# Optimization experiments

Hardware: AMD Instinct MI355X
Metric: run time of the kernel (lower is better)

The kernel has to match this reference:

```python
import jax, jax.numpy as jnp
import numpy as np

HEADS = 20  # head_dim = 1280 // 20 = 64
LORA_SCALE = 1.0


def setup_inputs() -> dict:
    key = jax.random.key(0)
    ks = jax.random.split(key, 16)
    B, S, C, R = 2, 2048, 1280, 4
    w = 0.02  # keep activations numerically tame
    inp = {
        "x": jax.random.normal(ks[0], (B, S, C), jnp.float32),
        "Wq": jax.random.normal(ks[1], (C, C), jnp.float32) * w,
        "Wk": jax.random.normal(ks[2], (C, C), jnp.float32) * w,
        "Wv": jax.random.normal(ks[3], (C, C), jnp.float32) * w,
        "Wo": jax.random.normal(ks[4], (C, C), jnp.float32) * w,
        "bo": jnp.zeros((C,), jnp.float32),
        "Aq": jax.random.normal(ks[5], (R, C), jnp.float32) * w,
        "Bq": jax.random.normal(ks[6], (C, R), jnp.float32) * w,
        "Ak": jax.random.normal(ks[7], (R, C), jnp.float32) * w,
        "Bk": jax.random.normal(ks[8], (C, R), jnp.float32) * w,
        "Av": jax.random.normal(ks[9], (R, C), jnp.float32) * w,
        "Bv": jax.random.normal(ks[10], (C, R), jnp.float32) * w,
        "Ao": jax.random.normal(ks[11], (R, C), jnp.float32) * w,
        "Bo": jax.random.normal(ks[12], (C, R), jnp.float32) * w,
    }
    return inp


def _lora(x, A, B):
    # LoRALinearLayer: up(down(x)); network_alpha=None -> no extra scaling
    return (x @ A.T) @ B.T


def reference(x, Wq, Wk, Wv, Wo, bo, Aq, Bq, Ak, Bk, Av, Bv, Ao, Bo):
    B, S, C = x.shape
    H = HEADS
    D = C // H
    # base projections + LoRA updates (self-attention: encoder_hidden_states = x)
    q = x @ Wq.T + LORA_SCALE * _lora(x, Aq, Bq)
    k = x @ Wk.T + LORA_SCALE * _lora(x, Ak, Bk)
    v = x @ Wv.T + LORA_SCALE * _lora(x, Av, Bv)
    # head split: [B, S, H, D]
    q = q.reshape(B, S, H, D)
    k = k.reshape(B, S, H, D)
    v = v.reshape(B, S, H, D)
    # explicit scores + softmax (attn.get_attention_scores), scale = 1/sqrt(D)
    scale = 1.0 / jnp.sqrt(jnp.asarray(D, x.dtype))
    scores = jnp.einsum("bshd,bthd->bhst", q, k) * scale  # [B, H, S, S]
    probs = jax.nn.softmax(scores, axis=-1)
    ctx = jnp.einsum("bhst,bthd->bshd", probs, v).reshape(B, S, C)
    # output projection (+bias) + LoRA; dropout is identity at eval
    out = ctx @ Wo.T + bo + LORA_SCALE * _lora(ctx, Ao, Bo)
    return out
```

## Files before the change

kernel.cpp:

```cpp
#include <hip/hip_runtime.h>

#define BATCH 2
#define SEQ   2048
#define CH    1280
#define NH    20
#define HD    64
#define BS    (BATCH*SEQ)
#define RK    4

typedef __attribute__((ext_vector_type(2)))  float floatx2;
typedef __attribute__((ext_vector_type(4)))  short bf16x4;
typedef __attribute__((ext_vector_type(8)))  short bf16x8;
typedef __attribute__((ext_vector_type(16))) float floatx16;

__device__ __forceinline__ floatx16 mfma32(bf16x8 a, bf16x8 b, floatx16 c) {
    return __builtin_amdgcn_mfma_f32_32x32x16_bf16(a, b, c, 0, 0, 0);
}
__device__ __forceinline__ floatx16 mfma32k8(bf16x4 a, bf16x4 b, floatx16 c) {
    return __builtin_amdgcn_mfma_f32_32x32x8bf16_1k(a, b, c, 0, 0, 0);
}

__device__ __forceinline__ unsigned short f2bf(float f) {
    unsigned int u = __float_as_uint(f);
    u += 0x7fffu + ((u >> 16) & 1u);
    return (unsigned short)(u >> 16);
}
__device__ __forceinline__ unsigned int packbf(float hi, float lo) {
    unsigned int a = __float_as_uint(hi) + 0x8000u;
    unsigned int b = __float_as_uint(lo) + 0x8000u;
    return __builtin_amdgcn_perm(a, b, 0x07060302u);
}
__device__ __forceinline__ float fexp2(float x) {
#if __has_builtin(__builtin_amdgcn_exp2f)
    return __builtin_amdgcn_exp2f(x);
#else
    return exp2f(x);
#endif
}

__device__ __forceinline__ void cp16(const unsigned short* g, unsigned short* l) {
    __builtin_amdgcn_global_load_lds(
        (const __attribute__((address_space(1))) unsigned int*)g,
        (__attribute__((address_space(3))) unsigned int*)l, 16, 0, 0);
}

#define FOLD_BLOCKS (CH * CH / 256)
#define CAST_BLOCKS (BS * CH / 1024)

__global__ __launch_bounds__(256) void prep(
    const float* __restrict__ x,
    const float* __restrict__ Wq, const float* __restrict__ Wk,
    const float* __restrict__ Wv, const float* __restrict__ Wo,
    const float* __restrict__ Aq, const float* __restrict__ Bq,
    const float* __restrict__ Ak, const float* __restrict__ Bk,
    const float* __restrict__ Av, const float* __restrict__ Bv,
    const float* __restrict__ Ao, const float* __restrict__ Bo,
    unsigned short* __restrict__ wq_bf, unsigned short* __restrict__ wk_bf,
    unsigned short* __restrict__ wv_bf, unsigned short* __restrict__ wo_bf,
    unsigned short* __restrict__ xb)
{
    const int bx = blockIdx.x;
    if (bx < 4 * FOLD_BLOCKS) {
        int which = bx / FOLD_BLOCKS;
        int e = (bx % FOLD_BLOCKS) * 256 + threadIdx.x;
        int i = e / CH, j = e % CH;
        const float *W, *A, *Bm;
        unsigned short* o;
        if (which == 0)      { W = Wq; A = Aq; Bm = Bq; o = wq_bf; }
        else if (which == 1) { W = Wk; A = Ak; Bm = Bk; o = wk_bf; }
        else if (which == 2) { W = Wv; A = Av; Bm = Bv; o = wv_bf; }
        else                 { W = Wo; A = Ao; Bm = Bo; o = wo_bf; }
        float acc = W[e];
#pragma unroll
        for (int r = 0; r < RK; r++) acc += Bm[i * RK + r] * A[r * CH + j];
        o[e] = f2bf(acc);
    } else {
        int idx = ((bx - 4 * FOLD_BLOCKS) * 256 + threadIdx.x) * 4;
        float4 v = *(const float4*)(x + idx);
        ushort4 o;
        o.x = f2bf(v.x); o.y = f2bf(v.y); o.z = f2bf(v.z); o.w = f2bf(v.w);
        *(ushort4*)(xb + idx) = o;
    }
}

template<bool OUTF>
__device__ __forceinline__ void gemm128(
    const unsigned short* __restrict__ A, const unsigned short* __restrict__ B,
    unsigned short* __restrict__ obf, float* __restrict__ of,
    const float* __restrict__ bias, float oscale)
{
    __shared__ __align__(16) unsigned short sa[128 * 64];
    __shared__ __align__(16) unsigned short sb[128 * 64];
    const int tid = threadIdx.x;
    const int wav = tid >> 6, lane = tid & 63;
    const int n32 = lane & 31, half = lane >> 5;
    const int wr = wav >> 1, wc = wav & 1;
    const int M0 = blockIdx.y * 128, N0 = blockIdx.x * 128;

    const unsigned short* ga[4]; const unsigned short* gb[4];
    unsigned short* la[4]; unsigned short* lb[4];
#pragma unroll
    for (int g = 0; g < 4; g++) {
        int s = g * 256 + tid;
        int row = s >> 3, cc = (s & 7) ^ (row & 7);
        ga[g] = A + (size_t)(M0 + row) * CH + cc * 8;
        gb[g] = B + (size_t)(N0 + row) * CH + cc * 8;
        la[g] = sa + (size_t)(g * 256 + wav * 64) * 8;
        lb[g] = sb + (size_t)(g * 256 + wav * 64) * 8;
    }

    const int arow0 = wr * 64 + n32, brow0 = wc * 64 + n32;

    floatx16 acc[2][2];
#pragma unroll
    for (int mt = 0; mt < 2; mt++)
#pragma unroll
        for (int nt = 0; nt < 2; nt++)
#pragma unroll
            for (int r = 0; r < 16; r++) acc[mt][nt][r] = 0.f;

    for (int k0 = 0; k0 < CH; k0 += 64) {
#pragma unroll
        for (int g = 0; g < 4; g++) { cp16(ga[g], la[g]); cp16(gb[g], lb[g]); }
#pragma unroll
        for (int g = 0; g < 4; g++) { ga[g] += 64; gb[g] += 64; }
        __syncthreads();

        bf16x8 av[2][4], bv[2][4];
#pragma unroll
        for (int mt = 0; mt < 2; mt++) {
            const int ar = arow0 + mt * 32, br = brow0 + mt * 32;
#pragma unroll
            for (int ks = 0; ks < 4; ks++) {
                const int cc = ks * 2 + half;
                av[mt][ks] = *(const bf16x8*)(sa + ar * 64 + ((cc ^ (ar & 7)) << 3));
                bv[mt][ks] = *(const bf16x8*)(sb + br * 64 + ((cc ^ (br & 7)) << 3));
            }
        }
#pragma unroll
        for (int ks = 0; ks < 4; ks++)
#pragma unroll
            for (int mt = 0; mt < 2; mt++)
#pragma unroll
                for (int nt = 0; nt < 2; nt++)
                    acc[mt][nt] = mfma32(av[mt][ks], bv[nt][ks], acc[mt][nt]);
        __syncthreads();
    }

#pragma unroll
    for (int mt = 0; mt < 2; mt++) {
#pragma unroll
        for (int nt = 0; nt < 2; nt++) {
            const int col = N0 + wc * 64 + nt * 32 + n32;
            const float bv2 = OUTF ? bias[col] : 0.f;
#pragma unroll
            for (int r = 0; r < 16; r++) {
                size_t row = (size_t)(M0 + wr * 64 + mt * 32 +
                                      (r & 3) + 8 * (r >> 2) + 4 * half);
                if (OUTF) of[row * CH + col] = acc[mt][nt][r] + bv2;
                else      obf[row * CH + col] = f2bf(acc[mt][nt][r] * oscale);
            }
        }
    }
}

__global__ __launch_bounds__(256) void gemm_qkv(
    const unsigned short* __restrict__ xb,
    const unsigned short* __restrict__ wq, const unsigned short* __restrict__ wk,
    const unsigned short* __restrict__ wv,
    unsigned short* __restrict__ q, unsigned short* __restrict__ k,
    unsigned short* __restrict__ v)
{
    const unsigned short* w = blockIdx.z == 0 ? wq : blockIdx.z == 1 ? wk : wv;
    unsigned short* o = blockIdx.z == 0 ? q : blockIdx.z == 1 ? k : v;
    float scale = blockIdx.z == 0 ? 0.18033688011112042f : 1.0f;
    gemm128<false>(xb, w, o, nullptr, nullptr, scale);
}

__global__ __launch_bounds__(256) void gemm_o(
    const unsigned short* __restrict__ c_bf, const unsigned short* __restrict__ wo,
    const float* __restrict__ bias, float* __restrict__ out)
{
    gemm128<true>(c_bf, wo, nullptr, out, bias, 1.0f);
}

__global__ __launch_bounds__(256) void transpose_v(
    const unsigned short* __restrict__ v, unsigned short* __restrict__ vt)
{
    __shared__ unsigned short lds[32][34];
    const int s0 = blockIdx.x * 32;
    const int d0 = blockIdx.y * 32;
    const int bh = blockIdx.z, b = bh / NH, h = bh % NH;
    const int c = threadIdx.x & 31;
    const int rbase = threadIdx.x >> 5;
#pragma unroll
    for (int i = 0; i < 4; i++) {
        int r = rbase + i * 8;
        lds[r][c] = v[(size_t)(b * SEQ + s0 + r) * CH + h * HD + d0 + c];
    }
    __syncthreads();
    const int cperm = (c & ~12) | ((c & 4) << 1) | ((c & 8) >> 1);
#pragma unroll
    for (int i = 0; i < 4; i++) {
        int r = rbase + i * 8;
        vt[(size_t)(bh * HD + d0 + r) * SEQ + s0 + cperm] = lds[c][r];
    }
}

__global__ __launch_bounds__(256, 4) void attention(
    const unsigned short* __restrict__ q, const unsigned short* __restrict__ k,
    const unsigned short* __restrict__ vt, unsigned short* __restrict__ c_bf)
{
    __shared__ __align__(16) unsigned short k_lds[128 * 64];
    __shared__ __align__(16) unsigned short v_lds[64 * 128];

    const int tid = threadIdx.x, wav = tid >> 6, lane = tid & 63;
    const int n32 = lane & 31, half = lane >> 5;
    const int q0 = blockIdx.x * 128;
    const int bh = blockIdx.y, b = bh / NH, h = bh % NH;

    const size_t qrow = (size_t)(b * SEQ + q0 + wav * 32 + n32);
    bf16x8 qf[4];
#pragma unroll
    for (int f = 0; f < 4; f++)
        qf[f] = *(const bf16x8*)(q + qrow * CH + h * HD + f * 16 + half * 8);

    const int rowk = tid >> 3, cck = (tid & 7) ^ (rowk & 7);
    const int rowv = tid >> 4, ccv = (tid & 15) ^ (rowv & 15);
    const unsigned short* gk0 = k + (size_t)(b * SEQ + rowk) * CH + h * HD + cck * 8;
    const unsigned short* gv0 = vt + (size_t)(bh * HD + rowv) * SEQ + ccv * 8;
    unsigned short* lk0 = k_lds + (size_t)(wav * 64) * 8;
    unsigned short* lv0 = v_lds + (size_t)(wav * 64) * 8;

    floatx2 ps = {0.f, 0.f};
    floatx16 acc[2];
#pragma unroll
    for (int dt = 0; dt < 2; dt++)
#pragma unroll
        for (int r = 0; r < 16; r++) acc[dt][r] = 0.f;

    for (int t0 = 0; t0 < SEQ; t0 += 128) {
#pragma unroll
        for (int g = 0; g < 4; g++) {
            cp16(gk0 + (size_t)g * 32 * CH, lk0 + g * 2048);
            cp16(gv0 + g * 16 * SEQ, lv0 + g * 2048);
        }
        gk0 += (size_t)128 * CH; gv0 += 128;
        __syncthreads();

#pragma unroll
        for (int kt = 0; kt < 4; kt++) {
            const int keyrow = kt * 32 + n32;
            const unsigned short* kr = k_lds + keyrow * 64;
            floatx16 st;
#pragma unroll
            for (int r = 0; r < 16; r++) st[r] = 0.f;
#pragma unroll
            for (int f = 0; f < 4; f++) {
                int phys = (2 * f + half) ^ (keyrow & 7);
                bf16x8 kf = *(const bf16x8*)(kr + phys * 8);
                st = mfma32(kf, qf[f], st);
            }

#pragma unroll
            for (int pp = 0; pp < 2; pp++) {
                float p[8];
#pragma unroll
                for (int r = 0; r < 8; r++) p[r] = fexp2(st[8 * pp + r]);
                unsigned int pk[4];
#pragma unroll
                for (int j = 0; j < 4; j++) {
                    ps += (floatx2){p[2 * j], p[2 * j + 1]};
                    pk[j] = packbf(p[2 * j + 1], p[2 * j]);
                }
                union { unsigned int u[2]; bf16x4 v; } pb0, pb1;
                pb0.u[0] = pk[0]; pb0.u[1] = pk[1];
                pb1.u[0] = pk[2]; pb1.u[1] = pk[3];
#pragma unroll
                for (int dt = 0; dt < 2; dt++) {
                    const int drow = dt * 32 + n32;
                    int ct = kt * 4 + pp * 2 + half;
                    int phys = ct ^ (drow & 15);
                    union { bf16x8 v8; bf16x4 v4[2]; } vv;
                    vv.v8 = *(const bf16x8*)(v_lds + drow * 128 + phys * 8);
                    acc[dt] = mfma32k8(vv.v4[0], pb0.v, acc[dt]);
                    acc[dt] = mfma32k8(vv.v4[1], pb1.v, acc[dt]);
                }
            }
        }
        __syncthreads();
    }

    float psum = ps.x + ps.y;
    float tot = psum + __shfl_xor(psum, 32, 64);
    float rinv = __frcp_rn(tot);
    const size_t obase = qrow * CH + h * HD;
#pragma unroll
    for (int dt = 0; dt < 2; dt++) {
#pragma unroll
        for (int jj = 0; jj < 4; jj++) {
            int d = dt * 32 + 8 * jj + 4 * half;
            uint2 o2;
            o2.x = packbf(acc[dt][4 * jj + 1] * rinv, acc[dt][4 * jj + 0] * rinv);
            o2.y = packbf(acc[dt][4 * jj + 3] * rinv, acc[dt][4 * jj + 2] * rinv);
            *(uint2*)(c_bf + obase + d) = o2;
        }
    }
}

extern "C" void kernel_launch(void* const* d_in, const int* in_sizes, int n_in,
                              void* d_out, int out_size, void* d_ws, size_t ws_size,
                              hipStream_t stream)
{
    const float* x  = (const float*)d_in[0];
    const float* Wq = (const float*)d_in[1];
    const float* Wk = (const float*)d_in[2];
    const float* Wv = (const float*)d_in[3];
    const float* Wo = (const float*)d_in[4];
    const float* bo = (const float*)d_in[5];
    const float* Aq = (const float*)d_in[6];
    const float* Bq = (const float*)d_in[7];
    const float* Ak = (const float*)d_in[8];
    const float* Bk = (const float*)d_in[9];
    const float* Av = (const float*)d_in[10];
    const float* Bv = (const float*)d_in[11];
    const float* Ao = (const float*)d_in[12];
    const float* Bo = (const float*)d_in[13];
    float* out = (float*)d_out;

    char* ws = (char*)d_ws;
    size_t off = 0;
    auto alloc = [&](size_t bytes) -> void* {
        void* p = ws + off; off += (bytes + 255) & ~(size_t)255; return p;
    };
    const size_t WB = (size_t)CH * CH, XB = (size_t)BS * CH;
    unsigned short* wq_bf = (unsigned short*)alloc(WB * 2);
    unsigned short* wk_bf = (unsigned short*)alloc(WB * 2);
    unsigned short* wv_bf = (unsigned short*)alloc(WB * 2);
    unsigned short* wo_bf = (unsigned short*)alloc(WB * 2);
    unsigned short* x_bf  = (unsigned short*)alloc(XB * 2);
    unsigned short* q_bf  = (unsigned short*)alloc(XB * 2);
    unsigned short* k_bf  = (unsigned short*)alloc(XB * 2);
    unsigned short* v_bf  = (unsigned short*)alloc(XB * 2);
    unsigned short* vt_bf = (unsigned short*)alloc(XB * 2);
    unsigned short* c_bf  = (unsigned short*)alloc(XB * 2);
    (void)ws_size; (void)n_in; (void)in_sizes; (void)out_size;

    prep<<<dim3(4 * FOLD_BLOCKS + CAST_BLOCKS), 256, 0, stream>>>(
        x, Wq, Wk, Wv, Wo, Aq, Bq, Ak, Bk, Av, Bv, Ao, Bo,
        wq_bf, wk_bf, wv_bf, wo_bf, x_bf);

    gemm_qkv<<<dim3(CH / 128, BS / 128, 3), 256, 0, stream>>>(
        x_bf, wq_bf, wk_bf, wv_bf, q_bf, k_bf, v_bf);

    transpose_v<<<dim3(SEQ / 32, 2, BATCH * NH), 256, 0, stream>>>(v_bf, vt_bf);

    attention<<<dim3(SEQ / 128, BATCH * NH), 256, 0, stream>>>(
        q_bf, k_bf, vt_bf, c_bf);

    gemm_o<<<dim3(CH / 128, BS / 128), 256, 0, stream>>>(c_bf, wo_bf, bo, out);
}
```

Baseline: 271.7 us.

## Fuse V transpose into QKV GEMM epilogue and vectorize weight folding

The V projection blocks of the QKV GEMM now stage their accumulator tile through shared memory and write V directly in the transposed, permuted layout that attention expects. This removes the separate transpose kernel, its launch, and one full round trip of V through global memory. The LoRA weight-fold prep is also vectorized to four elements per thread using float4 loads and ushort4 stores. The cost is a more complex epilogue with an extra barrier and a runtime mode branch in place of the compile-time template flag.

```diff
diff --git a/kernel.cpp b/kernel.cpp
--- a/kernel.cpp
+++ b/kernel.cpp
@@ -44,7 +44,7 @@
         (__attribute__((address_space(3))) unsigned int*)l, 16, 0, 0);
 }
 
-#define FOLD_BLOCKS (CH * CH / 256)
+#define F4_BLOCKS   (CH * CH / 1024)
 #define CAST_BLOCKS (BS * CH / 1024)
 
 __global__ __launch_bounds__(256) void prep(
@@ -60,9 +60,9 @@
     unsigned short* __restrict__ xb)
 {
     const int bx = blockIdx.x;
-    if (bx < 4 * FOLD_BLOCKS) {
-        int which = bx / FOLD_BLOCKS;
-        int e = (bx % FOLD_BLOCKS) * 256 + threadIdx.x;
+    if (bx < 4 * F4_BLOCKS) {
+        int which = bx / F4_BLOCKS;
+        int e = ((bx % F4_BLOCKS) * 256 + threadIdx.x) * 4;
         int i = e / CH, j = e % CH;
         const float *W, *A, *Bm;
         unsigned short* o;
@@ -70,12 +70,20 @@
         else if (which == 1) { W = Wk; A = Ak; Bm = Bk; o = wk_bf; }
         else if (which == 2) { W = Wv; A = Av; Bm = Bv; o = wv_bf; }
         else                 { W = Wo; A = Ao; Bm = Bo; o = wo_bf; }
-        float acc = W[e];
-#pragma unroll
-        for (int r = 0; r < RK; r++) acc += Bm[i * RK + r] * A[r * CH + j];
-        o[e] = f2bf(acc);
+        float4 acc = *(const float4*)(W + e);
+#pragma unroll
+        for (int r = 0; r < RK; r++) {
+            float bm = Bm[i * RK + r];
+            float4 a4 = *(const float4*)(A + r * CH + j);
+            acc.x += bm * a4.x; acc.y += bm * a4.y;
+            acc.z += bm * a4.z; acc.w += bm * a4.w;
+        }
+        ushort4 ov;
+        ov.x = f2bf(acc.x); ov.y = f2bf(acc.y);
+        ov.z = f2bf(acc.z); ov.w = f2bf(acc.w);
+        *(ushort4*)(o + e) = ov;
     } else {
-        int idx = ((bx - 4 * FOLD_BLOCKS) * 256 + threadIdx.x) * 4;
+        int idx = ((bx - 4 * F4_BLOCKS) * 256 + threadIdx.x) * 4;
         float4 v = *(const float4*)(x + idx);
         ushort4 o;
         o.x = f2bf(v.x); o.y = f2bf(v.y); o.z = f2bf(v.z); o.w = f2bf(v.w);
@@ -83,14 +91,15 @@
     }
 }
 
-template<bool OUTF>
 __device__ __forceinline__ void gemm128(
     const unsigned short* __restrict__ A, const unsigned short* __restrict__ B,
     unsigned short* __restrict__ obf, float* __restrict__ of,
-    const float* __restrict__ bias, float oscale)
-{
-    __shared__ __align__(16) unsigned short sa[128 * 64];
-    __shared__ __align__(16) unsigned short sb[128 * 64];
+    const float* __restrict__ bias, float oscale, int mode,
+    unsigned short* __restrict__ vt)
+{
+    __shared__ __align__(16) unsigned short smem[2 * 128 * 64];
+    unsigned short* sa = smem;
+    unsigned short* sb = smem + 128 * 64;
     const int tid = threadIdx.x;
     const int wav = tid >> 6, lane = tid & 63;
     const int n32 = lane & 31, half = lane >> 5;
@@ -147,18 +156,53 @@
         __syncthreads();
     }
 
+    if (mode == 2) {
+#pragma unroll
+        for (int mt = 0; mt < 2; mt++) {
+#pragma unroll
+            for (int nt = 0; nt < 2; nt++) {
+                const int dl = wc * 64 + nt * 32 + n32;
+#pragma unroll
+                for (int j = 0; j < 4; j++) {
+                    const int u = wr * 16 + mt * 8 + 2 * j + half;
+                    uint2 w;
+                    w.x = packbf(acc[mt][nt][4 * j + 1], acc[mt][nt][4 * j + 0]);
+                    w.y = packbf(acc[mt][nt][4 * j + 3], acc[mt][nt][4 * j + 2]);
+                    *(uint2*)(smem + dl * 128 + ((u ^ n32) << 2)) = w;
+                }
+            }
+        }
+        __syncthreads();
+        const int b = M0 >> 11;
+        const int s_in = M0 & (SEQ - 1);
+#pragma unroll
+        for (int g = 0; g < 8; g++) {
+            int cid = g * 256 + tid;
+            int dl = cid >> 4, pc = cid & 15;
+            int g32 = pc >> 2, p = (pc & 3) >> 1, hb = pc & 1;
+            int u1 = 8 * g32 + 4 * p + hb;
+            int sw = dl & 31;
+            uint2 r1 = *(const uint2*)(smem + dl * 128 + ((u1 ^ sw) << 2));
+            uint2 r2 = *(const uint2*)(smem + dl * 128 + (((u1 + 2) ^ sw) << 2));
+            int ch = N0 + dl, h = ch >> 6, d = ch & 63;
+            uint4 val; val.x = r1.x; val.y = r1.y; val.z = r2.x; val.w = r2.y;
+            *(uint4*)(vt + (size_t)((b * NH + h) * HD + d) * SEQ + s_in + pc * 8) = val;
+        }
+        return;
+    }
+
 #pragma unroll
     for (int mt = 0; mt < 2; mt++) {
 #pragma unroll
         for (int nt = 0; nt < 2; nt++) {
             const int col = N0 + wc * 64 + nt * 32 + n32;
-            const float bv2 = OUTF ? bias[col] : 0.f;
+            const float bv2 = (mode == 1) ? bias[col] : 0.f;
 #pragma unroll
             for (int r = 0; r < 16; r++) {
                 size_t row = (size_t)(M0 + wr * 64 + mt * 32 +
                                       (r & 3) + 8 * (r >> 2) + 4 * half);
-                if (OUTF) of[row * CH + col] = acc[mt][nt][r] + bv2;
-                else      obf[row * CH + col] = f2bf(acc[mt][nt][r] * oscale);
+                if (mode == 1) of[row * CH + col] = acc[mt][nt][r] + bv2;
+                else           obf[row * CH + col] = f2bf(acc[mt][nt][r] * oscale);
             }
         }
     }
@@ -169,42 +213,20 @@
     const unsigned short* __restrict__ wq, const unsigned short* __restrict__ wk,
     const unsigned short* __restrict__ wv,
     unsigned short* __restrict__ q, unsigned short* __restrict__ k,
-    unsigned short* __restrict__ v)
+    unsigned short* __restrict__ vt)
 {
     const unsigned short* w = blockIdx.z == 0 ? wq : blockIdx.z == 1 ? wk : wv;
-    unsigned short* o = blockIdx.z == 0 ? q : blockIdx.z == 1 ? k : v;
+    unsigned short* o = blockIdx.z == 0 ? q : k;
     float scale = blockIdx.z == 0 ? 0.18033688011112042f : 1.0f;
-    gemm128<false>(xb, w, o, nullptr, nullptr, scale);
+    int mode = blockIdx.z == 2 ? 2 : 0;
+    gemm128(xb, w, o, nullptr, nullptr, scale, mode, vt);
 }
 
 __global__ __launch_bounds__(256) void gemm_o(
     const unsigned short* __restrict__ c_bf, const unsigned short* __restrict__ wo,
     const float* __restrict__ bias, float* __restrict__ out)
 {
-    gemm128<true>(c_bf, wo, nullptr, out, bias, 1.0f);
-}
-
-__global__ __launch_bounds__(256) void transpose_v(
-    const unsigned short* __restrict__ v, unsigned short* __restrict__ vt)
-{
-    __shared__ unsigned short lds[32][34];
-    const int s0 = blockIdx.x * 32;
-    const int d0 = blockIdx.y * 32;
-    const int bh = blockIdx.z, b = bh / NH, h = bh % NH;
-    const int c = threadIdx.x & 31;
-    const int rbase = threadIdx.x >> 5;
-#pragma unroll
-    for (int i = 0; i < 4; i++) {
-        int r = rbase + i * 8;
-        lds[r][c] = v[(size_t)(b * SEQ + s0 + r) * CH + h * HD + d0 + c];
-    }
-    __syncthreads();
-    const int cperm = (c & ~12) | ((c & 4) << 1) | ((c & 8) >> 1);
-#pragma unroll
-    for (int i = 0; i < 4; i++) {
-        int r = rbase + i * 8;
-        vt[(size_t)(bh * HD + d0 + r) * SEQ + s0 + cperm] = lds[c][r];
-    }
+    gemm128(c_bf, wo, nullptr, out, bias, 1.0f, 1, nullptr);
 }
 
 __global__ __launch_bounds__(256, 4) void attention(
@@ -341,19 +363,16 @@
     unsigned short* x_bf  = (unsigned short*)alloc(XB * 2);
     unsigned short* q_bf  = (unsigned short*)alloc(XB * 2);
     unsigned short* k_bf  = (unsigned short*)alloc(XB * 2);
-    unsigned short* v_bf  = (unsigned short*)alloc(XB * 2);
     unsigned short* vt_bf = (unsigned short*)alloc(XB * 2);
     unsigned short* c_bf  = (unsigned short*)alloc(XB * 2);
     (void)ws_size; (void)n_in; (void)in_sizes; (void)out_size;
 
-    prep<<<dim3(4 * FOLD_BLOCKS + CAST_BLOCKS), 256, 0, stream>>>(
+    prep<<<dim3(4 * F4_BLOCKS + CAST_BLOCKS), 256, 0, stream>>>(
         x, Wq, Wk, Wv, Wo, Aq, Bq, Ak, Bk, Av, Bv, Ao, Bo,
         wq_bf, wk_bf, wv_bf, wo_bf, x_bf);
 
     gemm_qkv<<<dim3(CH / 128, BS / 128, 3), 256, 0, stream>>>(
-        x_bf, wq_bf, wk_bf, wv_bf, q_bf, k_bf, v_bf);
-
-    transpose_v<<<dim3(SEQ / 32, 2, BATCH * NH), 256, 0, stream>>>(v_bf, vt_bf);
+        x_bf, wq_bf, wk_bf, wv_bf, q_bf, k_bf, vt_bf);
 
     attention<<<dim3(SEQ / 128, BATCH * NH), 256, 0, stream>>>(
         q_bf, k_bf, vt_bf, c_bf);
```

After: 260.3 us. 1.04x faster.
